# Performance work log

Hardware: AMD Instinct MI355X
Metric: run time of the kernel (lower is better)

The kernel has to match this reference:

```python
import jax, jax.numpy as jnp
import numpy as np

IN_FEATURES = 1024
OUT_FEATURES = 64
DEGREE = 3
NUM_KNOTS = 10
BATCH = 8192
K0 = NUM_KNOTS + DEGREE  # number of basis columns / control points per edge


def b_spline_basis(x, knots, degree):
    """Vectorized Cox-de Boor recursion.
    x: (..., ) values in [0,1]; knots: (K0+1,).
    Returns (..., K0) basis; last `degree` columns are zero-padded (matches
    control_points width of num_knots+degree as in the original module).
    """
    t = knots
    n0 = t.shape[0] - 1  # = K0 degree-0 intervals
    xe = x[..., None]
    basis = ((xe >= t[:-1]) & (xe < t[1:])).astype(x.dtype)  # (..., K0)
    for p in range(1, degree + 1):
        ti = t[: n0 - p]
        tip = t[p:n0]
        ti1 = t[1 : n0 - p + 1]
        tip1 = t[p + 1 : n0 + 1]
        d1 = jnp.where(tip - ti > 0, tip - ti, jnp.ones_like(ti))
        d2 = jnp.where(tip1 - ti1 > 0, tip1 - ti1, jnp.ones_like(ti1))
        left = jnp.where(tip - ti > 0, (xe - ti) / d1, 0.0) * basis[..., : n0 - p]
        right = jnp.where(tip1 - ti1 > 0, (tip1 - xe) / d2, 0.0) * basis[..., 1 : n0 - p + 1]
        new = left + right
        pad = jnp.zeros(x.shape + (p,), x.dtype)
        basis = jnp.concatenate([new, pad], axis=-1)
    return basis


def setup_inputs() -> dict:
    key = jax.random.key(0)
    k1, k2 = jax.random.split(key)
    x = jax.random.uniform(k1, (BATCH, IN_FEATURES), dtype=jnp.float32)
    knots = jnp.linspace(0.0, 1.0, NUM_KNOTS + DEGREE + 1, dtype=jnp.float32)
    control_points = jax.random.normal(k2, (OUT_FEATURES, IN_FEATURES, K0), dtype=jnp.float32)
    return {"x": x, "knots": knots, "control_points": control_points}


def reference(x, knots, control_points):
    # basis: (B, in, K0) computed once per input feature (original recomputes
    # it out_features times inside a double loop -- same math, fused here).
    basis = b_spline_basis(x, knots, DEGREE)
    # outputs[b, o] = sum_j sum_k basis[b, j, k] * control_points[o, j, k]
    return jnp.einsum("bjk,ojk->bo", basis, control_points)
```

## Files before the change

### kernel.cpp

```cpp
#include <hip/hip_runtime.h>
#include <hip/hip_bf16.h>
#include <stdint.h>

#define IN_F   1024
#define OUT_F  64
#define BATCH  8192
#define BM     256
#define NTHR   512
#define JSPLIT 32
#define JPB    (IN_F / JSPLIT)
#define JC     4
#define NCH    (JPB / JC)
#define BT_B   (JC * 2048)
#define TBL_B  (14 * 32 * 48)
#define XSTG_B (BM * JPB * 4)
#define LDS_T  (TBL_B + XSTG_B + 2 * BT_B)
#define OUTSZ  (BATCH * OUT_F)

typedef __attribute__((ext_vector_type(8)))  short short8;
typedef __attribute__((ext_vector_type(16))) float f32x16;

__device__ __forceinline__ void gll16(const void* g, void* l) {
    __builtin_amdgcn_global_load_lds(
        (const __attribute__((address_space(1))) uint32_t*)g,
        (__attribute__((address_space(3))) uint32_t*)l,
        16, 0, 0);
}

__global__ void kan_prep(const float* __restrict__ cp, __hip_bfloat16* __restrict__ bt) {
    int j = blockIdx.x * 4 + (threadIdx.x >> 6);
    int o = threadIdx.x & 63;
    const float* src = cp + ((size_t)o * IN_F + j) * 13;
    float v[16];
#pragma unroll
    for (int k = 0; k < 10; ++k) v[k] = src[k];
#pragma unroll
    for (int k = 10; k < 16; ++k) v[k] = 0.0f;
    __hip_bfloat16* dst = bt + (size_t)j * 1024;
#pragma unroll
    for (int kh = 0; kh < 2; ++kh)
#pragma unroll
        for (int e = 0; e < 8; ++e)
            dst[kh * 512 + o * 8 + e] = __float2bfloat16(v[kh * 8 + e]);
}

template<bool PART>
__launch_bounds__(NTHR, 4)
__global__ void kan_main(const float* __restrict__ x,
                         const __hip_bfloat16* __restrict__ bt,
                         void* __restrict__ outp) {
    __shared__ __attribute__((aligned(16))) char lds[LDS_T];

    const int tid   = threadIdx.x;
    const int w     = tid >> 6;
    const int lane  = tid & 63;
    const int l31   = lane & 31;
    const int khalf = lane >> 5;

    const int r0 = blockIdx.x * BM;
    const int j0 = blockIdx.y * JPB;

    const char* btg = (const char*)bt + (size_t)j0 * 2048 + (size_t)tid * 16;
    const char* xlg = (const char*)x + ((size_t)(r0 + lane) * IN_F + j0) * 4;
    const int   wofs = w << 10;

#pragma unroll
    for (int i = 0; i < 4; ++i)
        gll16(xlg + (size_t)(i * 64) * 4096 + w * 16,
              lds + TBL_B + (w << 12) + (i << 10));

#define STAGE_BT(ch, bi) \
    gll16(btg + (size_t)(ch) * BT_B, lds + TBL_B + XSTG_B + (bi) * BT_B + wofs)

    STAGE_BT(0, 0);
    STAGE_BT(1, 1);

    for (int e = tid; e < 14 * 32; e += NTHR) {
        const int m = e >> 5, u5 = e & 31;
        const float uu = (u5 + 0.5f) * (1.0f / 32.0f);
        const float u2 = uu * uu;
        const float omu = 1.0f - uu;
        const float o2 = omu * omu;
        const float B3 = u2 * (uu * (1.0f / 6.0f));
        const float B0 = o2 * (omu * (1.0f / 6.0f));
        const float B1 = __builtin_fmaf(u2, __builtin_fmaf(uu, 0.5f, -1.0f), 2.0f / 3.0f);
        const float B2 = 1.0f - B0 - B1 - B3;
        uint32_t P01, P23;
        asm("v_cvt_pk_bf16_f32 %0, %1, %2" : "=v"(P01) : "v"(B0), "v"(B1));
        asm("v_cvt_pk_bf16_f32 %0, %1, %2" : "=v"(P23) : "v"(B2), "v"(B3));
        const uint64_t V = ((uint64_t)P23 << 32) | (uint64_t)P01;
#pragma unroll
        for (int h = 0; h < 2; ++h) {
            const int c0 = 48 + (h << 7);
            const int p = (m << 4) - c0;
            const uint64_t sl = V << ((uint32_t)p & 63);
            const uint64_t sr = V >> ((uint32_t)(-p) & 63);
            const uint64_t t0 = (p < 0) ? sr : sl;
            const uint64_t q0 = ((uint32_t)(p + 63) < 127u) ? t0 : 0ull;
            const uint64_t t1 = (p < 64) ? sr : sl;
            const uint64_t q1 = ((uint32_t)(p - 16) < 112u) ? t1 : 0ull;
            uint64_t* d = (uint64_t*)(lds + e * 48 + h * 16);
            d[0] = q0; d[1] = q1;
        }
    }

#define AFRAG(xv) ({                                              \
        const float t416_ = (xv) * 416.0f;           \
        const int i_ = (int)t416_;                 \
        const int s_ = ((i_ << 1) + i_) << 4;         \
        *(const short8*)(lds + s_ + (khalf << 4)); })

#define COMPUTE(ch, bi) do {                                                  \
        const char* base = lds + TBL_B + XSTG_B + (bi) * BT_B;                \
        float xa[4];                                                          \
        const char* xr = lds + TBL_B + (ch) * 4096 + (((w << 5) + l31) << 4); \
        *(float4*)xa = *(const float4*)(xr);    \
        const char* bbb = base + (khalf << 10) + l31 * 16;                    \
        _Pragma("unroll")                                                     \
        for (int jl = 0; jl < JC; ++jl) {                                     \
            const short8 b0 = *(const short8*)(bbb + jl * 2048);              \
            const short8 b1 = *(const short8*)(bbb + jl * 2048 + 512);        \
            const short8 a  = AFRAG(xa[jl]);                                  \
            acc0 = __builtin_amdgcn_mfma_f32_32x32x16_bf16(a, b0, acc0, 0, 0, 0); \
            acc1 = __builtin_amdgcn_mfma_f32_32x32x16_bf16(a, b1, acc1, 0, 0, 0); \
        }                                                                     \
    } while (0)

    f32x16 acc0, acc1;
#pragma unroll
    for (int i = 0; i < 16; ++i) { acc0[i] = 0.0f; acc1[i] = 0.0f; }

    __syncthreads();

    int cur = 0;
#pragma unroll 1
    for (int ch = 0; ch < NCH; ++ch) {
        if (ch >= 2) {
            if (ch == NCH - 1) asm volatile("s_waitcnt vmcnt(0)" ::: "memory");
            else               asm volatile("s_waitcnt vmcnt(1)" ::: "memory");
            __builtin_amdgcn_s_barrier();
            __builtin_amdgcn_sched_barrier(0);
        }
        COMPUTE(ch, cur);
        if (ch + 2 < NCH) {
            __builtin_amdgcn_s_barrier();
            __builtin_amdgcn_sched_barrier(0);
            STAGE_BT(ch + 2, cur);
        }
        cur ^= 1;
    }
#undef STAGE_BT
#undef AFRAG
#undef COMPUTE

    if (PART) {
        __hip_bfloat16* op = (__hip_bfloat16*)outp + (size_t)blockIdx.y * OUTSZ;
#pragma unroll
        for (int r = 0; r < 16; ++r) {
            const int crow = (r & 3) + 8 * (r >> 2) + 4 * khalf;
            __hip_bfloat16* p0 = op + (size_t)(r0 + (w << 5) + crow) * OUT_F;
            p0[l31]      = __float2bfloat16(acc0[r]);
            p0[l31 + 32] = __float2bfloat16(acc1[r]);
        }
    } else {
        float* op = (float*)outp;
#pragma unroll
        for (int r = 0; r < 16; ++r) {
            const int crow = (r & 3) + 8 * (r >> 2) + 4 * khalf;
            float* p0 = op + (size_t)(r0 + (w << 5) + crow) * OUT_F;
            atomicAdd(p0 + l31,      acc0[r]);
            atomicAdd(p0 + l31 + 32, acc1[r]);
        }
    }
}

__global__ void kan_reduce(const __hip_bfloat16* __restrict__ part,
                           float* __restrict__ out) {
    const int i = (blockIdx.x * 256 + threadIdx.x) * 8;
    float s[8] = {0, 0, 0, 0, 0, 0, 0, 0};
#pragma unroll
    for (int b = 0; b < JSPLIT; ++b) {
        const short8 v = *(const short8*)(part + (size_t)b * OUTSZ + i);
#pragma unroll
        for (int e = 0; e < 8; ++e) {
            union { uint32_t u; float f; } c;
            c.u = ((uint32_t)(uint16_t)v[e]) << 16;
            s[e] += c.f;
        }
    }
    float4 lo = {s[0], s[1], s[2], s[3]}, hi = {s[4], s[5], s[6], s[7]};
    *(float4*)(out + i)     = lo;
    *(float4*)(out + i + 4) = hi;
}

extern "C" void kernel_launch(void* const* d_in, const int* in_sizes, int n_in,
                              void* d_out, int out_size, void* d_ws, size_t ws_size,
                              hipStream_t stream) {
    const float* x  = (const float*)d_in[0];
    const float* cp = (const float*)d_in[2];
    float* out = (float*)d_out;
    __hip_bfloat16* bt   = (__hip_bfloat16*)d_ws;
    __hip_bfloat16* part = (__hip_bfloat16*)((char*)d_ws + 2u * 1024u * 1024u);

    const size_t need = 2u * 1024u * 1024u + (size_t)JSPLIT * OUTSZ * 2u;
    const bool use_part = ws_size >= need;

    kan_prep<<<dim3(IN_F / 4), dim3(256), 0, stream>>>(cp, bt);
    if (use_part) {
        kan_main<true><<<dim3(BATCH / BM, JSPLIT), dim3(NTHR), 0, stream>>>(x, bt, (void*)part);
        kan_reduce<<<dim3(OUTSZ / 2048), dim3(256), 0, stream>>>(part, out);
    } else {
        hipMemsetAsync(d_out, 0, (size_t)out_size * sizeof(float), stream);
        kan_main<false><<<dim3(BATCH / BM, JSPLIT), dim3(NTHR), 0, stream>>>(x, bt, (void*)d_out);
    }
}
```

Measured before the change: 41.02 us.

## Stage x in two halves, pad spline table, raise occupancy to six waves

The x tile is now staged into LDS in two 16KB halves. The second half is loaded mid-loop into the slots already consumed, which shrinks the LDS footprint so more blocks fit per CU. The launch bound's min-blocks hint rises from 4 to 6. The spline lookup table is re-laid out with padding every four entries, meant to reduce LDS bank conflicts on the per-lane gathered A-fragment reads. In exchange the second x load now sits inside the main loop, which adds a dependency on the vmcnt wait ordering, and the higher occupancy target may constrain register allocation.

```diff
diff --git a/kernel.cpp b/kernel.cpp
--- a/kernel.cpp
+++ b/kernel.cpp
@@ -12,9 +12,11 @@
 #define JC     4
 #define NCH    (JPB / JC)
 #define BT_B   (JC * 2048)
-#define TBL_B  (14 * 32 * 48)
-#define XSTG_B (BM * JPB * 4)
-#define LDS_T  (TBL_B + XSTG_B + 2 * BT_B)
+#define TBL_B  16128
+#define XSTG_B 16384
+#define XOFF   TBL_B
+#define BTOFF  (TBL_B + XSTG_B)
+#define LDS_T  (BTOFF + 2 * BT_B)
 #define OUTSZ  (BATCH * OUT_F)
 
 typedef __attribute__((ext_vector_type(8)))  short short8;
@@ -45,7 +47,7 @@
 }
 
 template<bool PART>
-__launch_bounds__(NTHR, 4)
+__launch_bounds__(NTHR, 6)
 __global__ void kan_main(const float* __restrict__ x,
                          const __hip_bfloat16* __restrict__ bt,
                          void* __restrict__ outp) {
@@ -61,17 +63,21 @@
     const int j0 = blockIdx.y * JPB;
 
     const char* btg = (const char*)bt + (size_t)j0 * 2048 + (size_t)tid * 16;
-    const char* xlg = (const char*)x + ((size_t)(r0 + lane) * IN_F + j0) * 4;
+    const char* xg  = (const char*)x +
+        (((size_t)(r0 + (tid & 255)) * IN_F + j0 + ((tid >> 8) << 2)) << 2);
     const int   wofs = w << 10;
 
-#pragma unroll
-    for (int i = 0; i < 4; ++i)
-        gll16(xlg + (size_t)(i * 64) * 4096 + w * 16,
-              lds + TBL_B + (w << 12) + (i << 10));
+#define XSTAGE(h) do {                                                        \
+        _Pragma("unroll")                                                     \
+        for (int k = 0; k < 2; ++k)                                           \
+            gll16(xg + ((h) * 4 + 2 * k) * 16,                                \
+                  lds + XOFF + ((2 * k + (w >> 2)) << 12) + ((w & 3) << 10)); \
+    } while (0)
 
 #define STAGE_BT(ch, bi) \
-    gll16(btg + (size_t)(ch) * BT_B, lds + TBL_B + XSTG_B + (bi) * BT_B + wofs)
-
+    gll16(btg + (size_t)(ch) * BT_B, lds + BTOFF + (bi) * BT_B + wofs)
+
+    XSTAGE(0);
     STAGE_BT(0, 0);
     STAGE_BT(1, 1);
 
@@ -89,6 +95,7 @@
         asm("v_cvt_pk_bf16_f32 %0, %1, %2" : "=v"(P01) : "v"(B0), "v"(B1));
         asm("v_cvt_pk_bf16_f32 %0, %1, %2" : "=v"(P23) : "v"(B2), "v"(B3));
         const uint64_t V = ((uint64_t)P23 << 32) | (uint64_t)P01;
+        const int ebase = (e >> 2) * 144 + ((e & 3) << 5);
 #pragma unroll
         for (int h = 0; h < 2; ++h) {
             const int c0 = 48 + (h << 7);
@@ -99,21 +106,21 @@
             const uint64_t q0 = ((uint32_t)(p + 63) < 127u) ? t0 : 0ull;
             const uint64_t t1 = (p < 64) ? sr : sl;
             const uint64_t q1 = ((uint32_t)(p - 16) < 112u) ? t1 : 0ull;
-            uint64_t* d = (uint64_t*)(lds + e * 48 + h * 16);
+            uint64_t* d = (uint64_t*)(lds + ebase + h * 16);
             d[0] = q0; d[1] = q1;
         }
     }
 
 #define AFRAG(xv) ({                                              \
-        const float t416_ = (xv) * 416.0f;           \
-        const int i_ = (int)t416_;                 \
-        const int s_ = ((i_ << 1) + i_) << 4;         \
-        *(const short8*)(lds + s_ + (khalf << 4)); })
+        const float t_ = (xv) * 416.0f;              \
+        const int i_ = (int)t_;                    \
+        const int a_ = (i_ >> 2) * 144 + ((i_ & 3) << 5) + (khalf << 4); \
+        *(const short8*)(lds + a_); })
 
 #define COMPUTE(ch, bi) do {                                                  \
-        const char* base = lds + TBL_B + XSTG_B + (bi) * BT_B;                \
+        const char* base = lds + BTOFF + (bi) * BT_B;                         \
         float xa[4];                                                          \
-        const char* xr = lds + TBL_B + (ch) * 4096 + (((w << 5) + l31) << 4); \
+        const char* xr = lds + XOFF + (((ch) & 3) << 12) + (((w << 5) + l31) << 4); \
         *(float4*)xa = *(const float4*)(xr);    \
         const char* bbb = base + (khalf << 10) + l31 * 16;                    \
         _Pragma("unroll")                                                     \
@@ -145,10 +152,12 @@
         if (ch + 2 < NCH) {
             __builtin_amdgcn_s_barrier();
             __builtin_amdgcn_sched_barrier(0);
+            if (ch == 3) XSTAGE(1);
             STAGE_BT(ch + 2, cur);
         }
         cur ^= 1;
     }
+#undef XSTAGE
 #undef STAGE_BT
 #undef AFRAG
 #undef COMPUTE
```

Result: slower. 42.82 us (+4.4%).
